# Optimization experiments

Hardware: AMD Instinct MI355X
Metric: run time of the kernel (lower is better)

## Reference

```python
import jax, jax.numpy as jnp
import numpy as np

B, T, D = 8, 2048, 1024
H, N = 8, 32  # n_heads, n_state


def _xavier(key, shape, fan_in, fan_out):
    lim = float(np.sqrt(6.0 / (fan_in + fan_out)))
    return jax.random.uniform(key, shape, jnp.float32, -lim, lim)


def setup_inputs() -> dict:
    key = jax.random.key(0)
    ks = jax.random.split(key, 8)
    x = jax.random.normal(ks[0], (B, T, D), jnp.float32)
    W_in = _xavier(ks[1], (D, D), D, D)                    # in_proj.weight [d_inner, dim]
    # per-head xavier on [n_state, d_inner] slices -> limit sqrt(6/(N+D))
    W_k = _xavier(ks[2], (H * N, D), N, D)
    W_v = _xavier(ks[3], (H * N, D), N, D)
    W_q = _xavier(ks[4], (H * N, D), N, D)
    W_beta = _xavier(ks[5], (H * N, D), N, D)
    b_beta = jnp.full((H, N), 2.0, jnp.float32)            # init_beta_bias
    W_out = _xavier(ks[6], (D, H * N), H * N, D)           # out_proj.weight [dim, H*n]
    return {"x": x, "W_in": W_in, "W_k": W_k, "W_v": W_v, "W_q": W_q,
            "W_beta": W_beta, "b_beta": b_beta, "W_out": W_out}


def reference(x, W_in, W_k, W_v, W_q, W_beta, b_beta, W_out):
    b, t, d = x.shape
    h, n = b_beta.shape
    # in_proj + SiLU (use_conv=False)
    xp = jax.nn.silu(jnp.einsum('btd,ed->bte', x, W_in))   # [B,T,D_inner]
    def proj(W):  # -> [T,B,H,N]
        return jnp.einsum('btd,md->btm', xp, W).reshape(b, t, h, n).transpose(1, 0, 2, 3)
    k_all = proj(W_k)
    v_all = proj(W_v)
    q_all = proj(W_q)
    beta_all = jax.nn.sigmoid(proj(W_beta) + b_beta)       # [T,B,H,N]

    S0 = jnp.zeros((b, h, n, n), x.dtype)

    def step(S, inp):
        k, v, q, beta = inp                                 # each [B,H,N]
        kn = k / (jnp.linalg.norm(k, axis=-1, keepdims=True) + 1e-6)
        retrieved = jnp.einsum('bhij,bhj->bhi', S, kn)
        delta = v - retrieved
        S = jnp.tanh(beta[..., None] * S + delta[..., None] * kn[..., None, :])
        Sq = jnp.einsum('bhij,bhj->bhi', S, q)
        out = Sq * jax.nn.silu(Sq)                          # [B,H,N]
        return S, out

    S_final, outs = jax.lax.scan(step, S0, (k_all, v_all, q_all, beta_all))
    cell_out = outs.transpose(1, 0, 2, 3).reshape(b, t, h * n)  # [B,T,H*N]
    y = jnp.einsum('btm,dm->btd', cell_out, W_out)          # out_proj, no bias
    return y, S_final
```

## Files before the change

kernel.cpp:

```cpp
#include <hip/hip_runtime.h>
#include <hip/hip_bf16.h>

#define TT 2048
#define BB 8
#define HH 8
#define NNS 32
#define MM (BB * TT)
#define CH 16

typedef __attribute__((ext_vector_type(8))) short short8;
typedef __attribute__((ext_vector_type(4))) float f32x4;

__device__ __forceinline__ float bf2f(ushort u) {
    return __uint_as_float(((unsigned)u) << 16);
}
__device__ __forceinline__ ushort f2bf(float f) {
    unsigned x = __float_as_uint(f);
    unsigned r = (x + 0x7fffu + ((x >> 16) & 1u)) >> 16;
    return (ushort)r;
}
__device__ __forceinline__ float sigmoidf_fast(float x) {
    float e = __builtin_amdgcn_exp2f(x * -1.4426950408889634f);
    return __builtin_amdgcn_rcpf(1.0f + e);
}
__device__ __forceinline__ float tanhf_fast(float x) {
    float e = __builtin_amdgcn_exp2f(x * 2.8853900817779268f);
    return fmaf(-2.0f, __builtin_amdgcn_rcpf(e + 1.0f), 1.0f);
}

template<int CTRL>
__device__ __forceinline__ float dpp_add(float x) {
    int y = __builtin_amdgcn_update_dpp(0, __float_as_int(x), CTRL, 0xF, 0xF, true);
    return x + __int_as_float(y);
}
__device__ __forceinline__ float red16(float x) {
    x = dpp_add<0xB1>(x);
    x = dpp_add<0x4E>(x);
    x = dpp_add<0x124>(x);
    x = dpp_add<0x128>(x);
    return x;
}

__device__ __forceinline__ void stage8_split(const float* __restrict__ src,
                                             ushort* __restrict__ hi,
                                             ushort* __restrict__ lo) {
    float4 x0 = *reinterpret_cast<const float4*>(src);
    float4 x1 = *reinterpret_cast<const float4*>(src + 4);
    float xs[8] = {x0.x, x0.y, x0.z, x0.w, x1.x, x1.y, x1.z, x1.w};
    ushort h[8], l[8];
#pragma unroll
    for (int i = 0; i < 8; ++i) {
        ushort hh = f2bf(xs[i]);
        h[i] = hh;
        l[i] = f2bf(xs[i] - bf2f(hh));
    }
    *reinterpret_cast<uint4*>(hi) = *reinterpret_cast<const uint4*>(h);
    *reinterpret_cast<uint4*>(lo) = *reinterpret_cast<const uint4*>(l);
}
__device__ __forceinline__ void stage8_hi(const float* __restrict__ src,
                                          ushort* __restrict__ hi) {
    float4 x0 = *reinterpret_cast<const float4*>(src);
    float4 x1 = *reinterpret_cast<const float4*>(src + 4);
    float xs[8] = {x0.x, x0.y, x0.z, x0.w, x1.x, x1.y, x1.z, x1.w};
    ushort h[8];
#pragma unroll
    for (int i = 0; i < 8; ++i) h[i] = f2bf(xs[i]);
    *reinterpret_cast<uint4*>(hi) = *reinterpret_cast<const uint4*>(h);
}

template<int ACT>
__global__ __launch_bounds__(256) void gemm_split(
    const float* __restrict__ A,
    const float* __restrict__ W0, const float* __restrict__ W1,
    const float* __restrict__ W2, const float* __restrict__ W3,
    const float* __restrict__ bbeta,
    float* __restrict__ C, int M, int N, int K)
{
    __shared__ __align__(16) ushort Ah[64][40], Al[64][40];
    __shared__ __align__(16) ushort Wh[64][40], Wl[64][40];
    const int n0 = blockIdx.x * 64;
    const int m0 = blockIdx.y * 64;
    const int t  = threadIdx.x;
    const int wave = t >> 6, lane = t & 63;
    const int lr = lane & 15, lq = lane >> 4;

    const float* Wsel;
    {
        int wi = n0 >> 8;
        Wsel = (wi == 0) ? W0 : (wi == 1) ? W1 : (wi == 2) ? W2 : W3;
    }
    const int wr0 = n0 & 255;
    const int ar = t >> 2;
    const int ak = (t & 3) * 8;

    f32x4 acc[4];
#pragma unroll
    for (int c = 0; c < 4; ++c) acc[c] = (f32x4){0.f, 0.f, 0.f, 0.f};

    for (int k0 = 0; k0 < K; k0 += 32) {
        __syncthreads();
        stage8_split(&A[(size_t)(m0 + ar) * K + k0 + ak], &Ah[ar][ak], &Al[ar][ak]);
        stage8_split(&Wsel[(size_t)(wr0 + ar) * K + k0 + ak], &Wh[ar][ak], &Wl[ar][ak]);
        __syncthreads();
        short8 ah = *reinterpret_cast<const short8*>(&Ah[wave * 16 + lr][lq * 8]);
        short8 al = *reinterpret_cast<const short8*>(&Al[wave * 16 + lr][lq * 8]);
#pragma unroll
        for (int c = 0; c < 4; ++c) {
            short8 bh = *reinterpret_cast<const short8*>(&Wh[c * 16 + lr][lq * 8]);
            short8 bl = *reinterpret_cast<const short8*>(&Wl[c * 16 + lr][lq * 8]);
            acc[c] = __builtin_amdgcn_mfma_f32_16x16x32_bf16(ah, bh, acc[c], 0, 0, 0);
            acc[c] = __builtin_amdgcn_mfma_f32_16x16x32_bf16(ah, bl, acc[c], 0, 0, 0);
            acc[c] = __builtin_amdgcn_mfma_f32_16x16x32_bf16(al, bh, acc[c], 0, 0, 0);
        }
    }

#pragma unroll
    for (int c = 0; c < 4; ++c) {
#pragma unroll
        for (int r2 = 0; r2 < 4; ++r2) {
            int mg = m0 + wave * 16 + lq * 4 + r2;
            int ng = n0 + c * 16 + lr;
            float v = acc[c][r2];
            if (ACT == 1) v = v * sigmoidf_fast(v);
            if (ACT == 2 && ng >= 768) v = sigmoidf_fast(v + bbeta[ng - 768]);
            C[(size_t)mg * N + ng] = v;
        }
    }
}

__global__ __launch_bounds__(256) void gemm_bf_a(
    const ushort* __restrict__ A,
    const float* __restrict__ W0, const float* __restrict__ W1,
    const float* __restrict__ W2, const float* __restrict__ W3,
    float* __restrict__ C, int M, int N, int K)
{
    __shared__ __align__(16) ushort As[64][40];
    __shared__ __align__(16) ushort Ws[64][40];
    const int n0 = blockIdx.x * 64;
    const int m0 = blockIdx.y * 64;
    const int t  = threadIdx.x;
    const int wave = t >> 6, lane = t & 63;
    const int lr = lane & 15, lq = lane >> 4;

    const float* Wsel;
    {
        int wi = n0 >> 8;
        Wsel = (wi == 0) ? W0 : (wi == 1) ? W1 : (wi == 2) ? W2 : W3;
    }
    const int wr0 = n0 & 255;
    const int ar = t >> 2;
    const int ak = (t & 3) * 8;

    f32x4 acc[4];
#pragma unroll
    for (int c = 0; c < 4; ++c) acc[c] = (f32x4){0.f, 0.f, 0.f, 0.f};

    for (int k0 = 0; k0 < K; k0 += 32) {
        __syncthreads();
        *reinterpret_cast<uint4*>(&As[ar][ak]) =
            *reinterpret_cast<const uint4*>(&A[(size_t)(m0 + ar) * K + k0 + ak]);
        stage8_hi(&Wsel[(size_t)(wr0 + ar) * K + k0 + ak], &Ws[ar][ak]);
        __syncthreads();
        short8 af = *reinterpret_cast<const short8*>(&As[wave * 16 + lr][lq * 8]);
#pragma unroll
        for (int c = 0; c < 4; ++c) {
            short8 bfv = *reinterpret_cast<const short8*>(&Ws[c * 16 + lr][lq * 8]);
            acc[c] = __builtin_amdgcn_mfma_f32_16x16x32_bf16(af, bfv, acc[c], 0, 0, 0);
        }
    }

#pragma unroll
    for (int c = 0; c < 4; ++c) {
#pragma unroll
        for (int r2 = 0; r2 < 4; ++r2) {
            int mg = m0 + wave * 16 + lq * 4 + r2;
            int ng = n0 + c * 16 + lr;
            C[(size_t)mg * N + ng] = acc[c][r2];
        }
    }
}

__global__ __launch_bounds__(256) void kn_kernel(
    const float* __restrict__ P, float* __restrict__ KN)
{
    int idx = blockIdx.x * 256 + threadIdx.x;
    int col = idx & 255;
    int bt  = idx >> 8;
    float k = P[(size_t)bt * 1024 + col];
    float ks = k * k;
    ks += __shfl_xor(ks, 1, 32);  ks += __shfl_xor(ks, 2, 32);
    ks += __shfl_xor(ks, 4, 32);  ks += __shfl_xor(ks, 8, 32);
    ks += __shfl_xor(ks, 16, 32);
    KN[idx] = k * __builtin_amdgcn_rcpf(sqrtf(ks) + 1e-6f);
}

__device__ __forceinline__ void lds_load8(
    float (&K_)[CH][32], float (&Q_)[CH][32], float (&VB)[CH][8],
    int base, int l, int iw,
    float (&k0)[8], float (&k1)[8], float (&q0)[8], float (&q1)[8],
    float (&vv)[8], float (&bb)[8])
{
#pragma unroll
    for (int u = 0; u < 8; ++u) {
        k0[u] = K_[base + u][l];  k1[u] = K_[base + u][l + 16];
        q0[u] = Q_[base + u][l];  q1[u] = Q_[base + u][l + 16];
        vv[u] = VB[base + u][iw]; bb[u] = VB[base + u][iw + 4];
    }
}

__device__ __forceinline__ void steps8(
    float (&k0)[8], float (&k1)[8], float (&q0)[8], float (&q1)[8],
    float (&vv)[8], float (&bb)[8],
    float& S0, float& S1, float (&sqp)[8])
{
#pragma unroll
    for (int u = 0; u < 8; ++u) {
        float p = red16(fmaf(S0, k0[u], S1 * k1[u]));
        float delta = vv[u] - p;
        S0 = tanhf_fast(fmaf(bb[u], S0, delta * k0[u]));
        S1 = tanhf_fast(fmaf(bb[u], S1, delta * k1[u]));
        sqp[u] = fmaf(S0, q0[u], S1 * q1[u]);
    }
}

__device__ __forceinline__ void flush8(
    float (&sqp)[8], ushort* __restrict__ cell, size_t crow, int l)
{
    float r0 = red16(sqp[0]), r1 = red16(sqp[1]);
    float r2 = red16(sqp[2]), r3 = red16(sqp[3]);
    float r4 = red16(sqp[4]), r5 = red16(sqp[5]);
    float r6 = red16(sqp[6]), r7 = red16(sqp[7]);
    if (l < 8) {
        float s01 = (l & 1) ? r1 : r0;
        float s23 = (l & 1) ? r3 : r2;
        float s45 = (l & 1) ? r5 : r4;
        float s67 = (l & 1) ? r7 : r6;
        float a03 = (l & 2) ? s23 : s01;
        float a47 = (l & 2) ? s67 : s45;
        float sel = (l & 4) ? a47 : a03;
        float o = sel * sel * sigmoidf_fast(sel);
        cell[crow + (size_t)l * 256] = f2bf(o);
    }
}

template<int DO_STAGE>
__device__ __forceinline__ void scan_chunk16(
    float (&K_)[CH][32], float (&Q_)[CH][32], float (&VB)[CH][8],
    float (&NK)[CH][32], float (&NQ)[CH][32], float (&NVB)[CH][8],
    const float*& gkn, const float*& gq, const float*& gv, const float*& gb,
    float (&k0A)[8], float (&k1A)[8], float (&q0A)[8], float (&q1A)[8],
    float (&vvA)[8], float (&bbA)[8],
    float (&k0B)[8], float (&k1B)[8], float (&q0B)[8], float (&q1B)[8],
    float (&vvB)[8], float (&bbB)[8],
    float& S0, float& S1, float (&sqp)[8],
    ushort* __restrict__ cell, size_t crow, int l, int iw, int j)
{
    float4 Lk0, Lk1, Lq0, Lq1;
    float Lv = 0.f, Lb = 0.f;
    if (DO_STAGE) {
        Lk0 = *reinterpret_cast<const float4*>(gkn);
        Lk1 = *reinterpret_cast<const float4*>(gkn + 8 * 256);
        Lq0 = *reinterpret_cast<const float4*>(gq);
        Lq1 = *reinterpret_cast<const float4*>(gq + 8 * 1024);
        Lv  = *gv;
        Lb  = *gb;
        gkn += CH * 256; gq += CH * 1024; gv += CH * 1024; gb += CH * 1024;
    }
    lds_load8(K_, Q_, VB, 8, l, iw, k0B, k1B, q0B, q1B, vvB, bbB);
    steps8(k0A, k1A, q0A, q1A, vvA, bbA, S0, S1, sqp);
    flush8(sqp, cell, crow, l);
    if (DO_STAGE) {
        *reinterpret_cast<float4*>(&NK[j >> 3][(j & 7) * 4]) = Lk0;
        *reinterpret_cast<float4*>(&NK[8 + (j >> 3)][(j & 7) * 4]) = Lk1;
        *reinterpret_cast<float4*>(&NQ[j >> 3][(j & 7) * 4]) = Lq0;
        *reinterpret_cast<float4*>(&NQ[8 + (j >> 3)][(j & 7) * 4]) = Lq1;
        NVB[j >> 2][j & 3] = Lv;
        NVB[j >> 2][4 + (j & 3)] = Lb;
        lds_load8(NK, NQ, NVB, 0, l, iw, k0A, k1A, q0A, q1A, vvA, bbA);
    }
    steps8(k0B, k1B, q0B, q1B, vvB, bbB, S0, S1, sqp);
    flush8(sqp, cell, crow + (size_t)8 * 256, l);
}

__global__ __launch_bounds__(64, 1) void scan_kernel(
    const float* __restrict__ P,
    const float* __restrict__ KN,
    ushort* __restrict__ cell,
    float* __restrict__ Sout)
{
    const int b    = blockIdx.x & 7;
    const int r    = blockIdx.x >> 3;
    const int h    = r & 7;
    const int quad = r >> 3;
    const int j    = threadIdx.x;
    const int l    = j & 15;
    const int iw   = j >> 4;
    const int i    = quad * 4 + iw;

    __shared__ __align__(16) float sK0[CH][32], sK1[CH][32];
    __shared__ __align__(16) float sQ0[CH][32], sQ1[CH][32];
    __shared__ __align__(16) float sVB0[CH][8], sVB1[CH][8];

    const size_t bt0 = (size_t)b * TT;
    const float* gkn = KN + (bt0 + (j >> 3)) * 256 + h * 32 + (j & 7) * 4;
    const float* gq  = P  + (bt0 + (j >> 3)) * 1024 + 512 + h * 32 + (j & 7) * 4;
    const float* gv  = P  + (bt0 + (j >> 2)) * 1024 + 256 + h * 32 + quad * 4 + (j & 3);
    const float* gb  = P  + (bt0 + (j >> 2)) * 1024 + 768 + h * 32 + quad * 4 + (j & 3);

    float k0A[8], k1A[8], q0A[8], q1A[8], vvA[8], bbA[8];
    float k0B[8], k1B[8], q0B[8], q1B[8], vvB[8], bbB[8];
    float sqp[8];
    float S0 = 0.f, S1 = 0.f;
    const size_t cb = (size_t)b * TT * 256 + h * 32 + i;

    {
        float4 K0v = *reinterpret_cast<const float4*>(gkn);
        float4 K1v = *reinterpret_cast<const float4*>(gkn + 8 * 256);
        float4 Q0v = *reinterpret_cast<const float4*>(gq);
        float4 Q1v = *reinterpret_cast<const float4*>(gq + 8 * 1024);
        float v0 = *gv, b0 = *gb;
        gkn += CH * 256; gq += CH * 1024; gv += CH * 1024; gb += CH * 1024;
        *reinterpret_cast<float4*>(&sK0[j >> 3][(j & 7) * 4]) = K0v;
        *reinterpret_cast<float4*>(&sK0[8 + (j >> 3)][(j & 7) * 4]) = K1v;
        *reinterpret_cast<float4*>(&sQ0[j >> 3][(j & 7) * 4]) = Q0v;
        *reinterpret_cast<float4*>(&sQ0[8 + (j >> 3)][(j & 7) * 4]) = Q1v;
        sVB0[j >> 2][j & 3] = v0;
        sVB0[j >> 2][4 + (j & 3)] = b0;
    }
    lds_load8(sK0, sQ0, sVB0, 0, l, iw, k0A, k1A, q0A, q1A, vvA, bbA);

    size_t crow = cb;
    for (int c = 0; c < 63; ++c) {
        scan_chunk16<1>(sK0, sQ0, sVB0, sK1, sQ1, sVB1,
                        gkn, gq, gv, gb,
                        k0A, k1A, q0A, q1A, vvA, bbA,
                        k0B, k1B, q0B, q1B, vvB, bbB,
                        S0, S1, sqp, cell, crow, l, iw, j);
        crow += (size_t)CH * 256;
        scan_chunk16<1>(sK1, sQ1, sVB1, sK0, sQ0, sVB0,
                        gkn, gq, gv, gb,
                        k0A, k1A, q0A, q1A, vvA, bbA,
                        k0B, k1B, q0B, q1B, vvB, bbB,
                        S0, S1, sqp, cell, crow, l, iw, j);
        crow += (size_t)CH * 256;
    }
    scan_chunk16<1>(sK0, sQ0, sVB0, sK1, sQ1, sVB1,
                    gkn, gq, gv, gb,
                    k0A, k1A, q0A, q1A, vvA, bbA,
                    k0B, k1B, q0B, q1B, vvB, bbB,
                    S0, S1, sqp, cell, crow, l, iw, j);
    crow += (size_t)CH * 256;
    scan_chunk16<0>(sK1, sQ1, sVB1, sK0, sQ0, sVB0,
                    gkn, gq, gv, gb,
                    k0A, k1A, q0A, q1A, vvA, bbA,
                    k0B, k1B, q0B, q1B, vvB, bbB,
                    S0, S1, sqp, cell, crow, l, iw, j);

    float* so = Sout + (((size_t)(b * HH + h)) * NNS + i) * NNS;
    so[l] = S0;
    so[l + 16] = S1;
}

extern "C" void kernel_launch(void* const* d_in, const int* in_sizes, int n_in,
                              void* d_out, int out_size, void* d_ws, size_t ws_size,
                              hipStream_t stream) {
    const float* x     = (const float*)d_in[0];
    const float* W_in  = (const float*)d_in[1];
    const float* W_k   = (const float*)d_in[2];
    const float* W_v   = (const float*)d_in[3];
    const float* W_q   = (const float*)d_in[4];
    const float* W_b   = (const float*)d_in[5];
    const float* b_b   = (const float*)d_in[6];
    const float* W_out = (const float*)d_in[7];
    float* out = (float*)d_out;

    const int M = MM;
    float*  xp   = (float*)d_ws;
    float*  P    = xp + (size_t)M * 1024;
    float*  KN   = P  + (size_t)M * 1024;
    ushort* cell = (ushort*)(KN + (size_t)M * 256);

    dim3 blk(256);
    dim3 g1(1024 / 64, M / 64);

    gemm_split<1><<<g1, blk, 0, stream>>>(x, W_in, W_in + 256 * 1024,
                                          W_in + 512 * 1024, W_in + 768 * 1024,
                                          b_b, xp, M, 1024, 1024);
    gemm_split<2><<<g1, blk, 0, stream>>>(xp, W_k, W_v, W_q, W_b,
                                          b_b, P, M, 1024, 1024);
    kn_kernel<<<dim3((M * 256) / 256), blk, 0, stream>>>(P, KN);
    scan_kernel<<<dim3(512), dim3(64), 0, stream>>>(P, KN, cell, out + (size_t)M * 1024);
    gemm_bf_a<<<g1, blk, 0, stream>>>(cell, W_out, W_out + 256 * 256,
                                      W_out + 512 * 256, W_out + 768 * 256,
                                      out, M, 1024, 256);
}
```

Before: 677.9 us.

## Enlarge GEMM block tiles to 128x128 with 2x2 wave layout and register blocking

```diff
diff --git a/kernel.cpp b/kernel.cpp
--- a/kernel.cpp
+++ b/kernel.cpp
@@ -76,13 +76,14 @@
     const float* __restrict__ bbeta,
     float* __restrict__ C, int M, int N, int K)
 {
-    __shared__ __align__(16) ushort Ah[64][40], Al[64][40];
-    __shared__ __align__(16) ushort Wh[64][40], Wl[64][40];
-    const int n0 = blockIdx.x * 64;
-    const int m0 = blockIdx.y * 64;
+    __shared__ __align__(16) ushort Ah[128][40], Al[128][40];
+    __shared__ __align__(16) ushort Wh[128][40], Wl[128][40];
+    const int n0 = blockIdx.x * 128;
+    const int m0 = blockIdx.y * 128;
     const int t  = threadIdx.x;
     const int wave = t >> 6, lane = t & 63;
     const int lr = lane & 15, lq = lane >> 4;
+    const int wm = wave >> 1, wn = wave & 1;
 
     const float* Wsel;
     {
@@ -90,40 +91,61 @@
         Wsel = (wi == 0) ? W0 : (wi == 1) ? W1 : (wi == 2) ? W2 : W3;
     }
     const int wr0 = n0 & 255;
-    const int ar = t >> 2;
-    const int ak = (t & 3) * 8;
-
-    f32x4 acc[4];
-#pragma unroll
-    for (int c = 0; c < 4; ++c) acc[c] = (f32x4){0.f, 0.f, 0.f, 0.f};
+    const int sr = t >> 1;
+    const int sc = (t & 1) * 16;
+
+    f32x4 acc[4][4];
+#pragma unroll
+    for (int mi = 0; mi < 4; ++mi)
+#pragma unroll
+        for (int ni = 0; ni < 4; ++ni) acc[mi][ni] = (f32x4){0.f, 0.f, 0.f, 0.f};
 
     for (int k0 = 0; k0 < K; k0 += 32) {
         __syncthreads();
-        stage8_split(&A[(size_t)(m0 + ar) * K + k0 + ak], &Ah[ar][ak], &Al[ar][ak]);
-        stage8_split(&Wsel[(size_t)(wr0 + ar) * K + k0 + ak], &Wh[ar][ak], &Wl[ar][ak]);
+        {
+            const float* as = &A[(size_t)(m0 + sr) * K + k0 + sc];
+            stage8_split(as,     &Ah[sr][sc],     &Al[sr][sc]);
+            stage8_split(as + 8, &Ah[sr][sc + 8], &Al[sr][sc + 8]);
+            const float* ws = &Wsel[(size_t)(wr0 + sr) * K + k0 + sc];
+            stage8_split(ws,     &Wh[sr][sc],     &Wl[sr][sc]);
+            stage8_split(ws + 8, &Wh[sr][sc + 8], &Wl[sr][sc + 8]);
+        }
         __syncthreads();
-        short8 ah = *reinterpret_cast<const short8*>(&Ah[wave * 16 + lr][lq * 8]);
-        short8 al = *reinterpret_cast<const short8*>(&Al[wave * 16 + lr][lq * 8]);
-#pragma unroll
-        for (int c = 0; c < 4; ++c) {
-            short8 bh = *reinterpret_cast<const short8*>(&Wh[c * 16 + lr][lq * 8]);
-            short8 bl = *reinterpret_cast<const short8*>(&Wl[c * 16 + lr][lq * 8]);
-            acc[c] = __builtin_amdgcn_mfma_f32_16x16x32_bf16(ah, bh, acc[c], 0, 0, 0);
-            acc[c] = __builtin_amdgcn_mfma_f32_16x16x32_bf16(ah, bl, acc[c], 0, 0, 0);
-            acc[c] = __builtin_amdgcn_mfma_f32_16x16x32_bf16(al, bh, acc[c], 0, 0, 0);
-        }
-    }
-
-#pragma unroll
-    for (int c = 0; c < 4; ++c) {
-#pragma unroll
-        for (int r2 = 0; r2 < 4; ++r2) {
-            int mg = m0 + wave * 16 + lq * 4 + r2;
-            int ng = n0 + c * 16 + lr;
-            float v = acc[c][r2];
-            if (ACT == 1) v = v * sigmoidf_fast(v);
-            if (ACT == 2 && ng >= 768) v = sigmoidf_fast(v + bbeta[ng - 768]);
-            C[(size_t)mg * N + ng] = v;
+        short8 ah[4], al[4], wh[4], wl[4];
+#pragma unroll
+        for (int mi = 0; mi < 4; ++mi) {
+            ah[mi] = *reinterpret_cast<const short8*>(&Ah[wm * 64 + mi * 16 + lr][lq * 8]);
+            al[mi] = *reinterpret_cast<const short8*>(&Al[wm * 64 + mi * 16 + lr][lq * 8]);
+        }
+#pragma unroll
+        for (int ni = 0; ni < 4; ++ni) {
+            wh[ni] = *reinterpret_cast<const short8*>(&Wh[wn * 64 + ni * 16 + lr][lq * 8]);
+            wl[ni] = *reinterpret_cast<const short8*>(&Wl[wn * 64 + ni * 16 + lr][lq * 8]);
+        }
+#pragma unroll
+        for (int mi = 0; mi < 4; ++mi) {
+#pragma unroll
+            for (int ni = 0; ni < 4; ++ni) {
+                acc[mi][ni] = __builtin_amdgcn_mfma_f32_16x16x32_bf16(ah[mi], wh[ni], acc[mi][ni], 0, 0, 0);
+                acc[mi][ni] = __builtin_amdgcn_mfma_f32_16x16x32_bf16(ah[mi], wl[ni], acc[mi][ni], 0, 0, 0);
+                acc[mi][ni] = __builtin_amdgcn_mfma_f32_16x16x32_bf16(al[mi], wh[ni], acc[mi][ni], 0, 0, 0);
+            }
+        }
+    }
+
+#pragma unroll
+    for (int mi = 0; mi < 4; ++mi) {
+#pragma unroll
+        for (int ni = 0; ni < 4; ++ni) {
+#pragma unroll
+            for (int r2 = 0; r2 < 4; ++r2) {
+                int mg = m0 + wm * 64 + mi * 16 + lq * 4 + r2;
+                int ng = n0 + wn * 64 + ni * 16 + lr;
+                float v = acc[mi][ni][r2];
+                if (ACT == 1) v = v * sigmoidf_fast(v);
+                if (ACT == 2 && ng >= 768) v = sigmoidf_fast(v + bbeta[ng - 768]);
+                C[(size_t)mg * N + ng] = v;
+            }
         }
     }
 }
@@ -134,13 +156,14 @@
     const float* __restrict__ W2, const float* __restrict__ W3,
     float* __restrict__ C, int M, int N, int K)
 {
-    __shared__ __align__(16) ushort As[64][40];
-    __shared__ __align__(16) ushort Ws[64][40];
-    const int n0 = blockIdx.x * 64;
-    const int m0 = blockIdx.y * 64;
+    __shared__ __align__(16) ushort As[128][40];
+    __shared__ __align__(16) ushort Ws[128][40];
+    const int n0 = blockIdx.x * 128;
+    const int m0 = blockIdx.y * 128;
     const int t  = threadIdx.x;
     const int wave = t >> 6, lane = t & 63;
     const int lr = lane & 15, lq = lane >> 4;
+    const int wm = wave >> 1, wn = wave & 1;
 
     const float* Wsel;
     {
@@ -148,34 +171,50 @@
         Wsel = (wi == 0) ? W0 : (wi == 1) ? W1 : (wi == 2) ? W2 : W3;
     }
     const int wr0 = n0 & 255;
-    const int ar = t >> 2;
-    const int ak = (t & 3) * 8;
-
-    f32x4 acc[4];
-#pragma unroll
-    for (int c = 0; c < 4; ++c) acc[c] = (f32x4){0.f, 0.f, 0.f, 0.f};
+    const int sr = t >> 1;
+    const int sc = (t & 1) * 16;
+
+    f32x4 acc[4][4];
+#pragma unroll
+    for (int mi = 0; mi < 4; ++mi)
+#pragma unroll
+        for (int ni = 0; ni < 4; ++ni) acc[mi][ni] = (f32x4){0.f, 0.f, 0.f, 0.f};
 
     for (int k0 = 0; k0 < K; k0 += 32) {
         __syncthreads();
-        *reinterpret_cast<uint4*>(&As[ar][ak]) =
-            *reinterpret_cast<const uint4*>(&A[(size_t)(m0 + ar) * K + k0 + ak]);
-        stage8_hi(&Wsel[(size_t)(wr0 + ar) * K + k0 + ak], &Ws[ar][ak]);
+        {
+            const ushort* as = &A[(size_t)(m0 + sr) * K + k0 + sc];
+            *reinterpret_cast<uint4*>(&As[sr][sc])     = *reinterpret_cast<const uint4*>(as);
+            *reinterpret_cast<uint4*>(&As[sr][sc + 8]) = *reinterpret_cast<const uint4*>(as + 8);
+            const float* ws = &Wsel[(size_t)(wr0 + sr) * K + k0 + sc];
+            stage8_hi(ws,     &Ws[sr][sc]);
+            stage8_hi(ws + 8, &Ws[sr][sc + 8]);
+        }
         __syncthreads();
-        short8 af = *reinterpret_cast<const short8*>(&As[wave * 16 + lr][lq * 8]);
-#pragma unroll
-        for (int c = 0; c < 4; ++c) {
-            short8 bfv = *reinterpret_cast<const short8*>(&Ws[c * 16 + lr][lq * 8]);
-            acc[c] = __builtin_amdgcn_mfma_f32_16x16x32_bf16(af, bfv, acc[c], 0, 0, 0);
-        }
-    }
-
-#pragma unroll
-    for (int c = 0; c < 4; ++c) {
-#pragma unroll
-        for (int r2 = 0; r2 < 4; ++r2) {
-            int mg = m0 + wave * 16 + lq * 4 + r2;
-            int ng = n0 + c * 16 + lr;
-            C[(size_t)mg * N + ng] = acc[c][r2];
+        short8 af[4], wf[4];
+#pragma unroll
+        for (int mi = 0; mi < 4; ++mi)
+            af[mi] = *reinterpret_cast<const short8*>(&As[wm * 64 + mi * 16 + lr][lq * 8]);
+#pragma unroll
+        for (int ni = 0; ni < 4; ++ni)
+            wf[ni] = *reinterpret_cast<const short8*>(&Ws[wn * 64 + ni * 16 + lr][lq * 8]);
+#pragma unroll
+        for (int mi = 0; mi < 4; ++mi)
+#pragma unroll
+            for (int ni = 0; ni < 4; ++ni)
+                acc[mi][ni] = __builtin_amdgcn_mfma_f32_16x16x32_bf16(af[mi], wf[ni], acc[mi][ni], 0, 0, 0);
+    }
+
+#pragma unroll
+    for (int mi = 0; mi < 4; ++mi) {
+#pragma unroll
+        for (int ni = 0; ni < 4; ++ni) {
+#pragma unroll
+            for (int r2 = 0; r2 < 4; ++r2) {
+                int mg = m0 + wm * 64 + mi * 16 + lq * 4 + r2;
+                int ng = n0 + wn * 64 + ni * 16 + lr;
+                C[(size_t)mg * N + ng] = acc[mi][ni][r2];
+            }
         }
     }
 }
@@ -381,7 +420,7 @@
     ushort* cell = (ushort*)(KN + (size_t)M * 256);
 
     dim3 blk(256);
-    dim3 g1(1024 / 64, M / 64);
+    dim3 g1(1024 / 128, M / 128);
 
     gemm_split<1><<<g1, blk, 0, stream>>>(x, W_in, W_in + 256 * 1024,
                                           W_in + 512 * 1024, W_in + 768 * 1024,
```

Measured after the change: 639.0 us. 5.7% less time.
